# Kernel tuning notes

Hardware: AMD Instinct MI355X
Metric: run time of the kernel (lower is better)

## Reference

```python
import jax, jax.numpy as jnp
import numpy as np

EPS = 1e-8


def _cdist(a, b):
    # a: [B,N,3], b: [B,M,3] -> euclidean distances [B,N,M]
    a2 = jnp.sum(a * a, axis=-1)[:, :, None]          # [B,N,1]
    b2 = jnp.sum(b * b, axis=-1)[:, None, :]          # [B,1,M]
    ab = jnp.einsum('bnd,bmd->bnm', a, b)             # [B,N,M]
    d2 = jnp.maximum(a2 + b2 - 2.0 * ab, 0.0)
    return jnp.sqrt(d2)


def setup_inputs() -> dict:
    key = jax.random.key(0)
    ks = jax.random.split(key, 8)
    B, N, M, C1, C2 = 16, 4096, 1024, 128, 256
    Cin = C1 + C2  # 384
    H1, H2 = 256, 128
    return {
        'xyz1': jax.random.normal(ks[0], (B, N, 3), dtype=jnp.float32),
        'xyz2': jax.random.normal(ks[1], (B, M, 3), dtype=jnp.float32),
        'points1': jax.random.normal(ks[2], (B, C1, N), dtype=jnp.float32),
        'points2': jax.random.normal(ks[3], (B, C2, M), dtype=jnp.float32),
        'W1': jax.random.normal(ks[4], (H1, Cin), dtype=jnp.float32) * (1.0 / np.sqrt(Cin)),
        'b1': jnp.zeros((H1,), dtype=jnp.float32),
        'W2': jax.random.normal(ks[5], (H2, H1), dtype=jnp.float32) * (1.0 / np.sqrt(H1)),
        'b2': jnp.zeros((H2,), dtype=jnp.float32),
    }


def reference(xyz1, xyz2, points1, points2, W1, b1, W2, b2):
    # inverse-distance weighted interpolation over ALL M source points
    dist = _cdist(xyz1, xyz2) + EPS                   # [B,N,M]
    inv = 1.0 / dist
    weight = inv / jnp.sum(inv, axis=-1, keepdims=True)
    # interpolated features: [B,N,M] @ [B,M,C2] -> [B,C2,N]
    interpolated = jnp.einsum('bnm,bcm->bcn', weight, points2)
    new_points = jnp.concatenate([points1, interpolated], axis=1)  # [B,C1+C2,N]
    # 1x1 Conv1d MLP with ReLU
    h = jax.nn.relu(jnp.einsum('oc,bcn->bon', W1, new_points) + b1[None, :, None])
    out = jax.nn.relu(jnp.einsum('oc,bcn->bon', W2, h) + b2[None, :, None])
    return out
```

## Files before the change

### kernel.cpp

```cpp
#include <hip/hip_runtime.h>
#include <math.h>

#define BBATCH 16
#define NPTS   4096
#define MPTS   1024
#define C1c    128
#define C2c    256
#define CINc   384
#define H1c    256
#define H2c    128
#define TN     64

typedef _Float16 f16x8 __attribute__((ext_vector_type(8)));
typedef _Float16 f16x4 __attribute__((ext_vector_type(4)));
typedef float    f32x4 __attribute__((ext_vector_type(4)));

#define INV_HALF   8192
#define OFF_XYZ2   32768
#define OFF_RED    49152
#define SMEM_BYTES 50176

#define NFRAG_P2  (BBATCH * 32 * 16 * 64)
#define NFRAG_W1  (16 * 12 * 64)
#define NFRAG_W2  (8 * 8 * 64)
#define WS_P2S  0
#define WS_W1S  (NFRAG_P2 * 8)
#define WS_W2S  (WS_W1S + NFRAG_W1 * 8)
#define WS_F16_TOTAL (WS_W2S + NFRAG_W2 * 8)

__global__ __launch_bounds__(256) void cvt_swz(
    const float* __restrict__ p2, const float* __restrict__ W1,
    const float* __restrict__ W2, _Float16* __restrict__ ws)
{
    const int t = blockIdx.x * 256 + threadIdx.x;
    const float* src;
    _Float16* dst;
    if (t < NFRAG_P2) {
        const int lane = t & 63, wt = (t >> 6) & 15, s = (t >> 10) & 31, b = t >> 15;
        const int c = wt * 16 + (lane & 15);
        const int m = s * 32 + (lane >> 4) * 8;
        src = p2 + ((size_t)(b * C2c + c)) * MPTS + m;
        dst = ws + WS_P2S + (size_t)t * 8;
    } else if (t < NFRAG_P2 + NFRAG_W1) {
        const int u = t - NFRAG_P2;
        const int lane = u & 63, kc = (u >> 6) % 12, wt = (u >> 6) / 12;
        const int o = wt * 16 + (lane & 15);
        const int k = kc * 32 + (lane >> 4) * 8;
        src = W1 + (size_t)o * CINc + k;
        dst = ws + WS_W1S + (size_t)u * 8;
    } else {
        const int v = t - NFRAG_P2 - NFRAG_W1;
        const int lane = v & 63, oc = (v >> 6) & 7, wt2 = v >> 9;
        const int o = wt2 * 16 + (lane & 15);
        const int k = oc * 32 + (lane >> 4) * 8;
        src = W2 + (size_t)o * H1c + k;
        dst = ws + WS_W2S + (size_t)v * 8;
    }
    const float4 a0 = *(const float4*)(src);
    const float4 a1 = *(const float4*)(src + 4);
    f16x8 h;
    h[0] = (_Float16)a0.x; h[1] = (_Float16)a0.y; h[2] = (_Float16)a0.z; h[3] = (_Float16)a0.w;
    h[4] = (_Float16)a1.x; h[5] = (_Float16)a1.y; h[6] = (_Float16)a1.z; h[7] = (_Float16)a1.w;
    *(f16x8*)dst = h;
}

template <bool F16P>
__global__ __launch_bounds__(256, 3) void fp_mfma9(
    const float* __restrict__ xyz1, const float* __restrict__ xyz2,
    const float* __restrict__ p1,   const float* __restrict__ p2,
    const float* __restrict__ W1,   const float* __restrict__ b1v,
    const float* __restrict__ W2,   const float* __restrict__ b2v,
    const _Float16* __restrict__ p2s, const _Float16* __restrict__ W1s,
    const _Float16* __restrict__ W2s,
    float* __restrict__ out)
{
    __shared__ __align__(16) char smem[SMEM_BYTES];
    _Float16* s_inv  = (_Float16*)smem;
    float*    s_xyz2 = (float*)(smem + OFF_XYZ2);
    _Float16* s_X    = (_Float16*)smem;
    _Float16* s_H    = (_Float16*)smem;
    float*    s_red  = (float*)(smem + OFF_RED);

    const int tid  = threadIdx.x;
    const int w    = tid >> 6;
    const int L    = tid & 63;
    const int quad = L >> 4;
    const int l16  = L & 15;

    const int id = blockIdx.x;
    const int b  = (id & 7) * 2 + ((id >> 3) & 1);
    const int n0 = (id >> 4) * TN;

    const float* __restrict__ z2b = xyz2 + (size_t)b * MPTS * 3;
    const float* __restrict__ p2b = p2   + (size_t)b * C2c * MPTS;
    const _Float16* __restrict__ p2sb =
        F16P ? (p2s + (((size_t)b * 32 * 16 + (size_t)w * 4) * 64 + L) * 8) : (const _Float16*)nullptr;

    for (int i = tid; i < MPTS * 3 / 4; i += 256)
        ((f32x4*)s_xyz2)[i] = ((const f32x4*)z2b)[i];

    const float x1x = xyz1[((size_t)b * NPTS + n0 + L) * 3 + 0];
    const float x1y = xyz1[((size_t)b * NPTS + n0 + L) * 3 + 1];
    const float x1z = xyz1[((size_t)b * NPTS + n0 + L) * 3 + 2];

    f32x4 acc[4][4];
    #pragma unroll
    for (int ct = 0; ct < 4; ++ct)
        #pragma unroll
        for (int nt = 0; nt < 4; ++nt)
            acc[ct][nt] = (f32x4){0.f, 0.f, 0.f, 0.f};

    float ssum = 0.f;
    f16x8 Aa[2][4];

    auto loadA = [&](int s, f16x8 dst[4]) {
        if (F16P) {
            const _Float16* ap = p2sb + (size_t)s * (16 * 64 * 8);
            #pragma unroll
            for (int ct = 0; ct < 4; ++ct)
                dst[ct] = *(const f16x8*)(ap + (size_t)ct * (64 * 8));
        } else {
            const float* ap = p2b + (size_t)(w * 64 + l16) * MPTS + s * 32 + quad * 8;
            #pragma unroll
            for (int ct = 0; ct < 4; ++ct) {
                const float4 a0 = *(const float4*)(ap + (size_t)ct * (16 * MPTS));
                const float4 a1 = *(const float4*)(ap + (size_t)ct * (16 * MPTS) + 4);
                f16x8 h;
                h[0] = (_Float16)a0.x; h[1] = (_Float16)a0.y; h[2] = (_Float16)a0.z; h[3] = (_Float16)a0.w;
                h[4] = (_Float16)a1.x; h[5] = (_Float16)a1.y; h[6] = (_Float16)a1.z; h[7] = (_Float16)a1.w;
                dst[ct] = h;
            }
        }
    };

    auto gen = [&](int ss_) {
        _Float16* buf = s_inv + (ss_ & 1) * INV_HALF;
        const float* zbase = s_xyz2 + (size_t)(ss_ * 128 + w * 32) * 3;
        #pragma unroll
        for (int g = 0; g < 4; ++g) {
            const float* zp = zbase + g * 24;
            f32x4 zr[6];
            #pragma unroll
            for (int j = 0; j < 6; ++j) zr[j] = ((const f32x4*)zp)[j];
            const float* zv = (const float*)zr;
            f16x8 iv;
            #pragma unroll
            for (int i = 0; i < 8; ++i) {
                const float dx = x1x - zv[3 * i + 0];
                const float dy = x1y - zv[3 * i + 1];
                const float dz = x1z - zv[3 * i + 2];
                const float d2 = fmaf(dx, dx, fmaf(dy, dy, fmaf(dz, dz, 1e-12f)));
                const float inv = __builtin_amdgcn_rsqf(d2);
                ssum += inv;
                iv[i] = (_Float16)inv;
            }
            *(f16x8*)(buf + (((w * 4 + quad) * 64) + g * 16 + l16) * 8) = iv;
        }
    };

    loadA(0, Aa[0]);
    __syncthreads();
    gen(0);
    __syncthreads();

    for (int ss = 0; ss < 8; ++ss) {
        if (ss + 1 < 8) gen(ss + 1);
        const _Float16* buf = s_inv + (ss & 1) * INV_HALF;
        #pragma unroll
        for (int cc = 0; cc < 4; ++cc) {
            const int s = ss * 4 + cc;
            if (s + 1 < 32) loadA(s + 1, Aa[(cc + 1) & 1]);
            __builtin_amdgcn_s_setprio(1);
            #pragma unroll
            for (int nt = 0; nt < 4; ++nt) {
                const f16x8 bf = *(const f16x8*)(buf + ((cc * 4 + nt) * 64 + L) * 8);
                #pragma unroll
                for (int ct = 0; ct < 4; ++ct)
                    acc[ct][nt] = __builtin_amdgcn_mfma_f32_16x16x32_f16(Aa[cc & 1][ct], bf, acc[ct][nt], 0, 0, 0);
            }
            __builtin_amdgcn_s_setprio(0);
        }
        __syncthreads();
    }

    {
        const float* p1b = p1 + ((size_t)b * C1c + w * 32 + quad * 8) * NPTS + n0 + l16;
        #pragma unroll
        for (int cc = 0; cc < 4; ++cc) {
            float t[8];
            #pragma unroll
            for (int j = 0; j < 8; ++j) t[j] = p1b[(size_t)j * NPTS + cc * 16];
            f16x8 v;
            #pragma unroll
            for (int j = 0; j < 8; ++j) v[j] = (_Float16)t[j];
            *(f16x8*)(s_X + ((w * 4 + cc) * 64 + L) * 8) = v;
        }
    }

    s_red[tid] = ssum;
    __syncthreads();
    if (tid < 64)
        s_red[tid] = 1.0f / (s_red[tid] + s_red[tid + 64] + s_red[tid + 128] + s_red[tid + 192]);
    __syncthreads();

    {
        float rn4[4];
        #pragma unroll
        for (int nt = 0; nt < 4; ++nt) rn4[nt] = s_red[nt * 16 + l16];
        #pragma unroll
        for (int ct = 0; ct < 4; ++ct) {
            const int kq = 4 + 2 * w + (ct >> 1);
            const int lp = l16 + 16 * (((ct & 1) * 2) + (quad >> 1));
            const int jo = (quad & 1) * 4;
            #pragma unroll
            for (int nt = 0; nt < 4; ++nt) {
                const f32x4 v = acc[ct][nt];
                const float r = rn4[nt];
                f16x4 hv;
                hv[0] = (_Float16)(v[0] * r);
                hv[1] = (_Float16)(v[1] * r);
                hv[2] = (_Float16)(v[2] * r);
                hv[3] = (_Float16)(v[3] * r);
                *(f16x4*)(s_X + ((kq * 4 + nt) * 64 + lp) * 8 + jo) = hv;
            }
        }
    }
    __syncthreads();

    f32x4 hacc[4][4];
    #pragma unroll
    for (int ct = 0; ct < 4; ++ct)
        #pragma unroll
        for (int nt = 0; nt < 4; ++nt)
            hacc[ct][nt] = (f32x4){0.f, 0.f, 0.f, 0.f};

    #pragma unroll 2
    for (int kc = 0; kc < 12; ++kc) {
        f16x8 af[4];
        if (F16P) {
            const _Float16* wp = W1s + (((size_t)(w * 4) * 12 + kc) * 64 + L) * 8;
            #pragma unroll
            for (int ct = 0; ct < 4; ++ct)
                af[ct] = *(const f16x8*)(wp + (size_t)ct * (12 * 64 * 8));
        } else {
            const float* wp = W1 + (size_t)(w * 64 + l16) * CINc + kc * 32 + quad * 8;
            #pragma unroll
            for (int ct = 0; ct < 4; ++ct) {
                const float4 a0 = *(const float4*)(wp + ct * (16 * CINc));
                const float4 a1 = *(const float4*)(wp + ct * (16 * CINc) + 4);
                f16x8 h;
                h[0] = (_Float16)a0.x; h[1] = (_Float16)a0.y; h[2] = (_Float16)a0.z; h[3] = (_Float16)a0.w;
                h[4] = (_Float16)a1.x; h[5] = (_Float16)a1.y; h[6] = (_Float16)a1.z; h[7] = (_Float16)a1.w;
                af[ct] = h;
            }
        }
        __builtin_amdgcn_s_setprio(1);
        #pragma unroll
        for (int nt = 0; nt < 4; ++nt) {
            const f16x8 bf = *(const f16x8*)(s_X + ((kc * 4 + nt) * 64 + L) * 8);
            #pragma unroll
            for (int ct = 0; ct < 4; ++ct)
                hacc[ct][nt] = __builtin_amdgcn_mfma_f32_16x16x32_f16(af[ct], bf, hacc[ct][nt], 0, 0, 0);
        }
        __builtin_amdgcn_s_setprio(0);
    }

    __syncthreads();

    {
        f32x4 bb[4];
        #pragma unroll
        for (int ct = 0; ct < 4; ++ct)
            bb[ct] = *(const f32x4*)(b1v + w * 64 + ct * 16 + quad * 4);
        #pragma unroll
        for (int ct = 0; ct < 4; ++ct) {
            const int oq = 2 * w + (ct >> 1);
            const int lp = l16 + 16 * (((ct & 1) * 2) + (quad >> 1));
            const int jo = (quad & 1) * 4;
            #pragma unroll
            for (int nt = 0; nt < 4; ++nt) {
                const f32x4 v = hacc[ct][nt];
                f16x4 hv;
                hv[0] = (_Float16)fmaxf(v[0] + bb[ct][0], 0.f);
                hv[1] = (_Float16)fmaxf(v[1] + bb[ct][1], 0.f);
                hv[2] = (_Float16)fmaxf(v[2] + bb[ct][2], 0.f);
                hv[3] = (_Float16)fmaxf(v[3] + bb[ct][3], 0.f);
                *(f16x4*)(s_H + ((oq * 4 + nt) * 64 + lp) * 8 + jo) = hv;
            }
        }
    }
    __syncthreads();

    f32x4 oacc[2][4];
    #pragma unroll
    for (int ct = 0; ct < 2; ++ct)
        #pragma unroll
        for (int nt = 0; nt < 4; ++nt)
            oacc[ct][nt] = (f32x4){0.f, 0.f, 0.f, 0.f};

    #pragma unroll 2
    for (int oc = 0; oc < 8; ++oc) {
        f16x8 af2[2];
        if (F16P) {
            const _Float16* wp = W2s + (((size_t)(w * 2) * 8 + oc) * 64 + L) * 8;
            #pragma unroll
            for (int ct = 0; ct < 2; ++ct)
                af2[ct] = *(const f16x8*)(wp + (size_t)ct * (8 * 64 * 8));
        } else {
            const float* wp = W2 + (size_t)(w * 32 + l16) * H1c + oc * 32 + quad * 8;
            #pragma unroll
            for (int ct = 0; ct < 2; ++ct) {
                const float4 a0 = *(const float4*)(wp + ct * (16 * H1c));
                const float4 a1 = *(const float4*)(wp + ct * (16 * H1c) + 4);
                f16x8 h;
                h[0] = (_Float16)a0.x; h[1] = (_Float16)a0.y; h[2] = (_Float16)a0.z; h[3] = (_Float16)a0.w;
                h[4] = (_Float16)a1.x; h[5] = (_Float16)a1.y; h[6] = (_Float16)a1.z; h[7] = (_Float16)a1.w;
                af2[ct] = h;
            }
        }
        __builtin_amdgcn_s_setprio(1);
        #pragma unroll
        for (int nt = 0; nt < 4; ++nt) {
            const f16x8 bf = *(const f16x8*)(s_H + ((oc * 4 + nt) * 64 + L) * 8);
            #pragma unroll
            for (int ct = 0; ct < 2; ++ct)
                oacc[ct][nt] = __builtin_amdgcn_mfma_f32_16x16x32_f16(af2[ct], bf, oacc[ct][nt], 0, 0, 0);
        }
        __builtin_amdgcn_s_setprio(0);
    }

    {
        f32x4 bb2[2];
        #pragma unroll
        for (int ct = 0; ct < 2; ++ct)
            bb2[ct] = *(const f32x4*)(b2v + w * 32 + ct * 16 + quad * 4);
        #pragma unroll
        for (int ct = 0; ct < 2; ++ct)
            #pragma unroll
            for (int nt = 0; nt < 4; ++nt) {
                float* op = out + ((size_t)b * H2c + w * 32 + ct * 16 + quad * 4) * NPTS
                                + n0 + nt * 16 + l16;
                #pragma unroll
                for (int j = 0; j < 4; ++j)
                    op[(size_t)j * NPTS] = fmaxf(oacc[ct][nt][j] + bb2[ct][j], 0.f);
            }
    }
}

extern "C" void kernel_launch(void* const* d_in, const int* in_sizes, int n_in,
                              void* d_out, int out_size, void* d_ws, size_t ws_size,
                              hipStream_t stream) {
    (void)in_sizes; (void)n_in; (void)out_size;
    const float* xyz1 = (const float*)d_in[0];
    const float* xyz2 = (const float*)d_in[1];
    const float* p1   = (const float*)d_in[2];
    const float* p2   = (const float*)d_in[3];
    const float* W1   = (const float*)d_in[4];
    const float* b1   = (const float*)d_in[5];
    const float* W2   = (const float*)d_in[6];
    const float* b2   = (const float*)d_in[7];
    float* out = (float*)d_out;

    dim3 grid(BBATCH * (NPTS / TN));
    dim3 block(256);
    if (ws_size >= (size_t)WS_F16_TOTAL * 2) {
        _Float16* ws = (_Float16*)d_ws;
        const int nswz = NFRAG_P2 + NFRAG_W1 + NFRAG_W2;
        cvt_swz<<<dim3(nswz / 256), dim3(256), 0, stream>>>(p2, W1, W2, ws);
        fp_mfma9<true><<<grid, block, 0, stream>>>(xyz1, xyz2, p1, p2, W1, b1, W2, b2,
                                                   ws + WS_P2S, ws + WS_W1S, ws + WS_W2S, out);
    } else {
        fp_mfma9<false><<<grid, block, 0, stream>>>(xyz1, xyz2, p1, p2, W1, b1, W2, b2,
                                                    nullptr, nullptr, nullptr, out);
    }
}
```

Baseline: 162.9 us.

## Process two point tiles per block with deeper prefetch and interleaved inverse-distance generation

Each block now handles two 64-point tiles in sequence, halving the grid and loading xyz2 into shared memory once per block. Shared memory moves xyz2 out of the region aliased by the X/H buffers so it survives across tiles. The p2 fragment prefetch depth goes from 2 to 4 buffers, inverse-distance generation for the next stage is split into per-chunk pieces interleaved with the MFMA loop, and W1/W2 fragment loads are double-buffered and fully unrolled. Occupancy drops from 3 to 2 blocks per CU, and the larger fragment buffers raise register pressure.

```diff
diff --git a/kernel.cpp b/kernel.cpp
--- a/kernel.cpp
+++ b/kernel.cpp
@@ -16,9 +16,9 @@
 typedef float    f32x4 __attribute__((ext_vector_type(4)));
 
 #define INV_HALF   8192
-#define OFF_XYZ2   32768
-#define OFF_RED    49152
-#define SMEM_BYTES 50176
+#define OFF_XYZ2   49152
+#define OFF_RED    61440
+#define SMEM_BYTES 62464
 
 #define NFRAG_P2  (BBATCH * 32 * 16 * 64)
 #define NFRAG_W1  (16 * 12 * 64)
@@ -65,7 +65,7 @@
 }
 
 template <bool F16P>
-__global__ __launch_bounds__(256, 3) void fp_mfma9(
+__global__ __launch_bounds__(256, 2) void fp_mfma10(
     const float* __restrict__ xyz1, const float* __restrict__ xyz2,
     const float* __restrict__ p1,   const float* __restrict__ p2,
     const float* __restrict__ W1,   const float* __restrict__ b1v,
@@ -76,9 +76,9 @@
 {
     __shared__ __align__(16) char smem[SMEM_BYTES];
     _Float16* s_inv  = (_Float16*)smem;
-    float*    s_xyz2 = (float*)(smem + OFF_XYZ2);
     _Float16* s_X    = (_Float16*)smem;
     _Float16* s_H    = (_Float16*)smem;
+    float*    s_xyz2 = (float*)(smem + OFF_XYZ2);
     float*    s_red  = (float*)(smem + OFF_RED);
 
     const int tid  = threadIdx.x;
@@ -89,7 +89,7 @@
 
     const int id = blockIdx.x;
     const int b  = (id & 7) * 2 + ((id >> 3) & 1);
-    const int n0 = (id >> 4) * TN;
+    const int n0base = (id >> 4) * (2 * TN);
 
     const float* __restrict__ z2b = xyz2 + (size_t)b * MPTS * 3;
     const float* __restrict__ p2b = p2   + (size_t)b * C2c * MPTS;
@@ -98,20 +98,6 @@
 
     for (int i = tid; i < MPTS * 3 / 4; i += 256)
         ((f32x4*)s_xyz2)[i] = ((const f32x4*)z2b)[i];
-
-    const float x1x = xyz1[((size_t)b * NPTS + n0 + L) * 3 + 0];
-    const float x1y = xyz1[((size_t)b * NPTS + n0 + L) * 3 + 1];
-    const float x1z = xyz1[((size_t)b * NPTS + n0 + L) * 3 + 2];
-
-    f32x4 acc[4][4];
-    #pragma unroll
-    for (int ct = 0; ct < 4; ++ct)
-        #pragma unroll
-        for (int nt = 0; nt < 4; ++nt)
-            acc[ct][nt] = (f32x4){0.f, 0.f, 0.f, 0.f};
-
-    float ssum = 0.f;
-    f16x8 Aa[2][4];
 
     auto loadA = [&](int s, f16x8 dst[4]) {
         if (F16P) {
@@ -133,12 +119,66 @@
         }
     };
 
-    auto gen = [&](int ss_) {
-        _Float16* buf = s_inv + (ss_ & 1) * INV_HALF;
-        const float* zbase = s_xyz2 + (size_t)(ss_ * 128 + w * 32) * 3;
+    auto loadW1 = [&](int kc, f16x8 dst[4]) {
+        if (F16P) {
+            const _Float16* wp = W1s + (((size_t)(w * 4) * 12 + kc) * 64 + L) * 8;
+            #pragma unroll
+            for (int ct = 0; ct < 4; ++ct)
+                dst[ct] = *(const f16x8*)(wp + (size_t)ct * (12 * 64 * 8));
+        } else {
+            const float* wp = W1 + (size_t)(w * 64 + l16) * CINc + kc * 32 + quad * 8;
+            #pragma unroll
+            for (int ct = 0; ct < 4; ++ct) {
+                const float4 a0 = *(const float4*)(wp + ct * (16 * CINc));
+                const float4 a1 = *(const float4*)(wp + ct * (16 * CINc) + 4);
+                f16x8 h;
+                h[0] = (_Float16)a0.x; h[1] = (_Float16)a0.y; h[2] = (_Float16)a0.z; h[3] = (_Float16)a0.w;
+                h[4] = (_Float16)a1.x; h[5] = (_Float16)a1.y; h[6] = (_Float16)a1.z; h[7] = (_Float16)a1.w;
+                dst[ct] = h;
+            }
+        }
+    };
+
+    auto loadW2 = [&](int oc, f16x8 dst[2]) {
+        if (F16P) {
+            const _Float16* wp = W2s + (((size_t)(w * 2) * 8 + oc) * 64 + L) * 8;
+            #pragma unroll
+            for (int ct = 0; ct < 2; ++ct)
+                dst[ct] = *(const f16x8*)(wp + (size_t)ct * (8 * 64 * 8));
+        } else {
+            const float* wp = W2 + (size_t)(w * 32 + l16) * H1c + oc * 32 + quad * 8;
+            #pragma unroll
+            for (int ct = 0; ct < 2; ++ct) {
+                const float4 a0 = *(const float4*)(wp + ct * (16 * H1c));
+                const float4 a1 = *(const float4*)(wp + ct * (16 * H1c) + 4);
+                f16x8 h;
+                h[0] = (_Float16)a0.x; h[1] = (_Float16)a0.y; h[2] = (_Float16)a0.z; h[3] = (_Float16)a0.w;
+                h[4] = (_Float16)a1.x; h[5] = (_Float16)a1.y; h[6] = (_Float16)a1.z; h[7] = (_Float16)a1.w;
+                dst[ct] = h;
+            }
+        }
+    };
+
+    for (int t = 0; t < 2; ++t) {
+        const int n0 = n0base + t * TN;
+
+        const float x1x = xyz1[((size_t)b * NPTS + n0 + L) * 3 + 0];
+        const float x1y = xyz1[((size_t)b * NPTS + n0 + L) * 3 + 1];
+        const float x1z = xyz1[((size_t)b * NPTS + n0 + L) * 3 + 2];
+
+        f32x4 acc[4][4];
         #pragma unroll
-        for (int g = 0; g < 4; ++g) {
-            const float* zp = zbase + g * 24;
+        for (int ct = 0; ct < 4; ++ct)
+            #pragma unroll
+            for (int nt = 0; nt < 4; ++nt)
+                acc[ct][nt] = (f32x4){0.f, 0.f, 0.f, 0.f};
+
+        float ssum = 0.f;
+        f16x8 Aa[4][4];
+
+        auto gen_g = [&](int ss_, int g) {
+            _Float16* buf = s_inv + (ss_ & 1) * INV_HALF;
+            const float* zp = s_xyz2 + (size_t)(ss_ * 128 + w * 32 + g * 8) * 3;
             f32x4 zr[6];
             #pragma unroll
             for (int j = 0; j < 6; ++j) zr[j] = ((const f32x4*)zp)[j];
@@ -155,195 +195,171 @@
                 iv[i] = (_Float16)inv;
             }
             *(f16x8*)(buf + (((w * 4 + quad) * 64) + g * 16 + l16) * 8) = iv;
-        }
-    };
-
-    loadA(0, Aa[0]);
-    __syncthreads();
-    gen(0);
-    __syncthreads();
-
-    for (int ss = 0; ss < 8; ++ss) {
-        if (ss + 1 < 8) gen(ss + 1);
-        const _Float16* buf = s_inv + (ss & 1) * INV_HALF;
+        };
+
+        loadA(0, Aa[0]);
+        loadA(1, Aa[1]);
+        __syncthreads();
         #pragma unroll
-        for (int cc = 0; cc < 4; ++cc) {
-            const int s = ss * 4 + cc;
-            if (s + 1 < 32) loadA(s + 1, Aa[(cc + 1) & 1]);
-            __builtin_amdgcn_s_setprio(1);
-            #pragma unroll
-            for (int nt = 0; nt < 4; ++nt) {
-                const f16x8 bf = *(const f16x8*)(buf + ((cc * 4 + nt) * 64 + L) * 8);
-                #pragma unroll
-                for (int ct = 0; ct < 4; ++ct)
-                    acc[ct][nt] = __builtin_amdgcn_mfma_f32_16x16x32_f16(Aa[cc & 1][ct], bf, acc[ct][nt], 0, 0, 0);
-            }
-            __builtin_amdgcn_s_setprio(0);
-        }
-        __syncthreads();
-    }
-
-    {
-        const float* p1b = p1 + ((size_t)b * C1c + w * 32 + quad * 8) * NPTS + n0 + l16;
-        #pragma unroll
-        for (int cc = 0; cc < 4; ++cc) {
-            float t[8];
-            #pragma unroll
-            for (int j = 0; j < 8; ++j) t[j] = p1b[(size_t)j * NPTS + cc * 16];
-            f16x8 v;
-            #pragma unroll
-            for (int j = 0; j < 8; ++j) v[j] = (_Float16)t[j];
-            *(f16x8*)(s_X + ((w * 4 + cc) * 64 + L) * 8) = v;
-        }
-    }
-
-    s_red[tid] = ssum;
-    __syncthreads();
-    if (tid < 64)
-        s_red[tid] = 1.0f / (s_red[tid] + s_red[tid + 64] + s_red[tid + 128] + s_red[tid + 192]);
-    __syncthreads();
-
-    {
-        float rn4[4];
-        #pragma unroll
-        for (int nt = 0; nt < 4; ++nt) rn4[nt] = s_red[nt * 16 + l16];
-        #pragma unroll
-        for (int ct = 0; ct < 4; ++ct) {
-            const int kq = 4 + 2 * w + (ct >> 1);
-            const int lp = l16 + 16 * (((ct & 1) * 2) + (quad >> 1));
-            const int jo = (quad & 1) * 4;
-            #pragma unroll
-            for (int nt = 0; nt < 4; ++nt) {
-                const f32x4 v = acc[ct][nt];
-                const float r = rn4[nt];
-                f16x4 hv;
-                hv[0] = (_Float16)(v[0] * r);
-                hv[1] = (_Float16)(v[1] * r);
-                hv[2] = (_Float16)(v[2] * r);
-                hv[3] = (_Float16)(v[3] * r);
-                *(f16x4*)(s_X + ((kq * 4 + nt) * 64 + lp) * 8 + jo) = hv;
-            }
-        }
-    }
-    __syncthreads();
-
-    f32x4 hacc[4][4];
-    #pragma unroll
-    for (int ct = 0; ct < 4; ++ct)
-        #pragma unroll
-        for (int nt = 0; nt < 4; ++nt)
-            hacc[ct][nt] = (f32x4){0.f, 0.f, 0.f, 0.f};
-
-    #pragma unroll 2
-    for (int kc = 0; kc < 12; ++kc) {
-        f16x8 af[4];
-        if (F16P) {
-            const _Float16* wp = W1s + (((size_t)(w * 4) * 12 + kc) * 64 + L) * 8;
-            #pragma unroll
-            for (int ct = 0; ct < 4; ++ct)
-                af[ct] = *(const f16x8*)(wp + (size_t)ct * (12 * 64 * 8));
-        } else {
-            const float* wp = W1 + (size_t)(w * 64 + l16) * CINc + kc * 32 + quad * 8;
+        for (int g = 0; g < 4; ++g) gen_g(0, g);
+        __syncthreads();
+
+        for (int ss = 0; ss < 8; ++ss) {
+            const _Float16* buf = s_inv + (ss & 1) * INV_HALF;
+            #pragma unroll
+            for (int cc = 0; cc < 4; ++cc) {
+                const int s = ss * 4 + cc;
+                if (s + 2 < 32) loadA(s + 2, Aa[(cc + 2) & 3]);
+                if (ss + 1 < 8) gen_g(ss + 1, cc);
+                __builtin_amdgcn_s_setprio(1);
+                #pragma unroll
+                for (int nt = 0; nt < 4; ++nt) {
+                    const f16x8 bf = *(const f16x8*)(buf + ((cc * 4 + nt) * 64 + L) * 8);
+                    #pragma unroll
+                    for (int ct = 0; ct < 4; ++ct)
+                        acc[ct][nt] = __builtin_amdgcn_mfma_f32_16x16x32_f16(Aa[cc][ct], bf, acc[ct][nt], 0, 0, 0);
+                }
+                __builtin_amdgcn_s_setprio(0);
+            }
+            __syncthreads();
+        }
+
+        {
+            const float* p1b = p1 + ((size_t)b * C1c + w * 32 + quad * 8) * NPTS + n0 + l16;
+            #pragma unroll
+            for (int cc = 0; cc < 4; ++cc) {
+                float tv[8];
+                #pragma unroll
+                for (int j = 0; j < 8; ++j) tv[j] = p1b[(size_t)j * NPTS + cc * 16];
+                f16x8 v;
+                #pragma unroll
+                for (int j = 0; j < 8; ++j) v[j] = (_Float16)tv[j];
+                *(f16x8*)(s_X + ((w * 4 + cc) * 64 + L) * 8) = v;
+            }
+        }
+
+        s_red[tid] = ssum;
+        __syncthreads();
+        if (tid < 64)
+            s_red[tid] = 1.0f / (s_red[tid] + s_red[tid + 64] + s_red[tid + 128] + s_red[tid + 192]);
+        __syncthreads();
+
+        {
+            float rn4[4];
+            #pragma unroll
+            for (int nt = 0; nt < 4; ++nt) rn4[nt] = s_red[nt * 16 + l16];
             #pragma unroll
             for (int ct = 0; ct < 4; ++ct) {
-                const float4 a0 = *(const float4*)(wp + ct * (16 * CINc));
-                const float4 a1 = *(const float4*)(wp + ct * (16 * CINc) + 4);
-                f16x8 h;
-                h[0] = (_Float16)a0.x; h[1] = (_Float16)a0.y; h[2] = (_Float16)a0.z; h[3] = (_Float16)a0.w;
-                h[4] = (_Float16)a1.x; h[5] = (_Float16)a1.y; h[6] = (_Float16)a1.z; h[7] = (_Float16)a1.w;
-                af[ct] = h;
-            }
-        }
-        __builtin_amdgcn_s_setprio(1);
-        #pragma unroll
-        for (int nt = 0; nt < 4; ++nt) {
-            const f16x8 bf = *(const f16x8*)(s_X + ((kc * 4 + nt) * 64 + L) * 8);
-            #pragma unroll
-            for (int ct = 0; ct < 4; ++ct)
-                hacc[ct][nt] = __builtin_amdgcn_mfma_f32_16x16x32_f16(af[ct], bf, hacc[ct][nt], 0, 0, 0);
-        }
-        __builtin_amdgcn_s_setprio(0);
-    }
-
-    __syncthreads();
-
-    {
-        f32x4 bb[4];
+                const int kq = 4 + 2 * w + (ct >> 1);
+                const int lp = l16 + 16 * (((ct & 1) * 2) + (quad >> 1));
+                const int jo = (quad & 1) * 4;
+                #pragma unroll
+                for (int nt = 0; nt < 4; ++nt) {
+                    const f32x4 v = acc[ct][nt];
+                    const float r = rn4[nt];
+                    f16x4 hv;
+                    hv[0] = (_Float16)(v[0] * r);
+                    hv[1] = (_Float16)(v[1] * r);
+                    hv[2] = (_Float16)(v[2] * r);
+                    hv[3] = (_Float16)(v[3] * r);
+                    *(f16x4*)(s_X + ((kq * 4 + nt) * 64 + lp) * 8 + jo) = hv;
+                }
+            }
+        }
+        __syncthreads();
+
+        f32x4 hacc[4][4];
         #pragma unroll
         for (int ct = 0; ct < 4; ++ct)
-            bb[ct] = *(const f32x4*)(b1v + w * 64 + ct * 16 + quad * 4);
-        #pragma unroll
-        for (int ct = 0; ct < 4; ++ct) {
-            const int oq = 2 * w + (ct >> 1);
-            const int lp = l16 + 16 * (((ct & 1) * 2) + (quad >> 1));
-            const int jo = (quad & 1) * 4;
-            #pragma unroll
-            for (int nt = 0; nt < 4; ++nt) {
-                const f32x4 v = hacc[ct][nt];
-                f16x4 hv;
-                hv[0] = (_Float16)fmaxf(v[0] + bb[ct][0], 0.f);
-                hv[1] = (_Float16)fmaxf(v[1] + bb[ct][1], 0.f);
-                hv[2] = (_Float16)fmaxf(v[2] + bb[ct][2], 0.f);
-                hv[3] = (_Float16)fmaxf(v[3] + bb[ct][3], 0.f);
-                *(f16x4*)(s_H + ((oq * 4 + nt) * 64 + lp) * 8 + jo) = hv;
-            }
-        }
-    }
-    __syncthreads();
-
-    f32x4 oacc[2][4];
-    #pragma unroll
-    for (int ct = 0; ct < 2; ++ct)
-        #pragma unroll
-        for (int nt = 0; nt < 4; ++nt)
-            oacc[ct][nt] = (f32x4){0.f, 0.f, 0.f, 0.f};
-
-    #pragma unroll 2
-    for (int oc = 0; oc < 8; ++oc) {
-        f16x8 af2[2];
-        if (F16P) {
-            const _Float16* wp = W2s + (((size_t)(w * 2) * 8 + oc) * 64 + L) * 8;
-            #pragma unroll
-            for (int ct = 0; ct < 2; ++ct)
-                af2[ct] = *(const f16x8*)(wp + (size_t)ct * (8 * 64 * 8));
-        } else {
-            const float* wp = W2 + (size_t)(w * 32 + l16) * H1c + oc * 32 + quad * 8;
-            #pragma unroll
-            for (int ct = 0; ct < 2; ++ct) {
-                const float4 a0 = *(const float4*)(wp + ct * (16 * H1c));
-                const float4 a1 = *(const float4*)(wp + ct * (16 * H1c) + 4);
-                f16x8 h;
-                h[0] = (_Float16)a0.x; h[1] = (_Float16)a0.y; h[2] = (_Float16)a0.z; h[3] = (_Float16)a0.w;
-                h[4] = (_Float16)a1.x; h[5] = (_Float16)a1.y; h[6] = (_Float16)a1.z; h[7] = (_Float16)a1.w;
-                af2[ct] = h;
-            }
-        }
-        __builtin_amdgcn_s_setprio(1);
-        #pragma unroll
-        for (int nt = 0; nt < 4; ++nt) {
-            const f16x8 bf = *(const f16x8*)(s_H + ((oc * 4 + nt) * 64 + L) * 8);
-            #pragma unroll
-            for (int ct = 0; ct < 2; ++ct)
-                oacc[ct][nt] = __builtin_amdgcn_mfma_f32_16x16x32_f16(af2[ct], bf, oacc[ct][nt], 0, 0, 0);
-        }
-        __builtin_amdgcn_s_setprio(0);
-    }
-
-    {
-        f32x4 bb2[2];
+            #pragma unroll
+            for (int nt = 0; nt < 4; ++nt)
+                hacc[ct][nt] = (f32x4){0.f, 0.f, 0.f, 0.f};
+
+        {
+            f16x8 afP[2][4];
+            loadW1(0, afP[0]);
+            #pragma unroll
+            for (int kc = 0; kc < 12; ++kc) {
+                if (kc + 1 < 12) loadW1(kc + 1, afP[(kc + 1) & 1]);
+                __builtin_amdgcn_s_setprio(1);
+                #pragma unroll
+                for (int nt = 0; nt < 4; ++nt) {
+                    const f16x8 bf = *(const f16x8*)(s_X + ((kc * 4 + nt) * 64 + L) * 8);
+                    #pragma unroll
+                    for (int ct = 0; ct < 4; ++ct)
+                        hacc[ct][nt] = __builtin_amdgcn_mfma_f32_16x16x32_f16(afP[kc & 1][ct], bf, hacc[ct][nt], 0, 0, 0);
+                }
+                __builtin_amdgcn_s_setprio(0);
+            }
+        }
+
+        __syncthreads();
+
+        {
+            f32x4 bb[4];
+            #pragma unroll
+            for (int ct = 0; ct < 4; ++ct)
+                bb[ct] = *(const f32x4*)(b1v + w * 64 + ct * 16 + quad * 4);
+            #pragma unroll
+            for (int ct = 0; ct < 4; ++ct) {
+                const int oq = 2 * w + (ct >> 1);
+                const int lp = l16 + 16 * (((ct & 1) * 2) + (quad >> 1));
+                const int jo = (quad & 1) * 4;
+                #pragma unroll
+                for (int nt = 0; nt < 4; ++nt) {
+                    const f32x4 v = hacc[ct][nt];
+                    f16x4 hv;
+                    hv[0] = (_Float16)fmaxf(v[0] + bb[ct][0], 0.f);
+                    hv[1] = (_Float16)fmaxf(v[1] + bb[ct][1], 0.f);
+                    hv[2] = (_Float16)fmaxf(v[2] + bb[ct][2], 0.f);
+                    hv[3] = (_Float16)fmaxf(v[3] + bb[ct][3], 0.f);
+                    *(f16x4*)(s_H + ((oq * 4 + nt) * 64 + lp) * 8 + jo) = hv;
+                }
+            }
+        }
+        __syncthreads();
+
+        f32x4 oacc[2][4];
         #pragma unroll
         for (int ct = 0; ct < 2; ++ct)
-            bb2[ct] = *(const f32x4*)(b2v + w * 32 + ct * 16 + quad * 4);
-        #pragma unroll
-        for (int ct = 0; ct < 2; ++ct)
-            #pragma unroll
-            for (int nt = 0; nt < 4; ++nt) {
-                float* op = out + ((size_t)b * H2c + w * 32 + ct * 16 + quad * 4) * NPTS
-                                + n0 + nt * 16 + l16;
-                #pragma unroll
-                for (int j = 0; j < 4; ++j)
-                    op[(size_t)j * NPTS] = fmaxf(oacc[ct][nt][j] + bb2[ct][j], 0.f);
-            }
+            #pragma unroll
+            for (int nt = 0; nt < 4; ++nt)
+                oacc[ct][nt] = (f32x4){0.f, 0.f, 0.f, 0.f};
+
+        {
+            f16x8 afP2[2][2];
+            loadW2(0, afP2[0]);
+            #pragma unroll
+            for (int oc = 0; oc < 8; ++oc) {
+                if (oc + 1 < 8) loadW2(oc + 1, afP2[(oc + 1) & 1]);
+                __builtin_amdgcn_s_setprio(1);
+                #pragma unroll
+                for (int nt = 0; nt < 4; ++nt) {
+                    const f16x8 bf = *(const f16x8*)(s_H + ((oc * 4 + nt) * 64 + L) * 8);
+                    #pragma unroll
+                    for (int ct = 0; ct < 2; ++ct)
+                        oacc[ct][nt] = __builtin_amdgcn_mfma_f32_16x16x32_f16(afP2[oc & 1][ct], bf, oacc[ct][nt], 0, 0, 0);
+                }
+                __builtin_amdgcn_s_setprio(0);
+            }
+        }
+
+        {
+            f32x4 bb2[2];
+            #pragma unroll
+            for (int ct = 0; ct < 2; ++ct)
+                bb2[ct] = *(const f32x4*)(b2v + w * 32 + ct * 16 + quad * 4);
+            #pragma unroll
+            for (int ct = 0; ct < 2; ++ct)
+                #pragma unroll
+                for (int nt = 0; nt < 4; ++nt) {
+                    float* op = out + ((size_t)b * H2c + w * 32 + ct * 16 + quad * 4) * NPTS
+                                    + n0 + nt * 16 + l16;
+                    #pragma unroll
+                    for (int j = 0; j < 4; ++j)
+                        op[(size_t)j * NPTS] = fmaxf(oacc[ct][nt][j] + bb2[ct][j], 0.f);
+                }
+        }
     }
 }
 
@@ -361,16 +377,16 @@
     const float* b2   = (const float*)d_in[7];
     float* out = (float*)d_out;
 
-    dim3 grid(BBATCH * (NPTS / TN));
+    dim3 grid(BBATCH * (NPTS / TN) / 2);
     dim3 block(256);
     if (ws_size >= (size_t)WS_F16_TOTAL * 2) {
         _Float16* ws = (_Float16*)d_ws;
         const int nswz = NFRAG_P2 + NFRAG_W1 + NFRAG_W2;
         cvt_swz<<<dim3(nswz / 256), dim3(256), 0, stream>>>(p2, W1, W2, ws);
-        fp_mfma9<true><<<grid, block, 0, stream>>>(xyz1, xyz2, p1, p2, W1, b1, W2, b2,
-                                                   ws + WS_P2S, ws + WS_W1S, ws + WS_W2S, out);
+        fp_mfma10<true><<<grid, block, 0, stream>>>(xyz1, xyz2, p1, p2, W1, b1, W2, b2,
+                                                    ws + WS_P2S, ws + WS_W1S, ws + WS_W2S, out);
     } else {
-        fp_mfma9<false><<<grid, block, 0, stream>>>(xyz1, xyz2, p1, p2, W1, b1, W2, b2,
-                                                    nullptr, nullptr, nullptr, out);
+        fp_mfma10<false><<<grid, block, 0, stream>>>(xyz1, xyz2, p1, p2, W1, b1, W2, b2,
+                                                     nullptr, nullptr, nullptr, out);
     }
 }
```

Result: slower. 216.5 us (+32.9%).
